# Optimization experiments

Hardware: AMD Instinct MI355X
Metric: run time of the kernel (lower is better)

## Reference

```python
import jax, jax.numpy as jnp
import numpy as np

B, S, E = 2, 2048, 1024
H, BLK = 16, 32
HD = E // H


def setup_inputs() -> dict:
    key = jax.random.key(0)
    ks = jax.random.split(key, 9)
    s = 1.0 / np.sqrt(E)
    return {
        "x": jax.random.normal(ks[0], (B, S, E), dtype=jnp.float32),
        "Wq": jax.random.normal(ks[1], (E, E), dtype=jnp.float32) * s,
        "bq": jnp.zeros((E,), dtype=jnp.float32),
        "Wk": jax.random.normal(ks[2], (E, E), dtype=jnp.float32) * s,
        "bk": jnp.zeros((E,), dtype=jnp.float32),
        "Wv": jax.random.normal(ks[3], (E, E), dtype=jnp.float32) * s,
        "bv": jnp.zeros((E,), dtype=jnp.float32),
        "Wo": jax.random.normal(ks[4], (E, E), dtype=jnp.float32) * s,
        "bo": jnp.zeros((E,), dtype=jnp.float32),
    }


def reference(x, Wq, bq, Wk, bk, Wv, bv, Wo, bo):
    b, s, e = x.shape
    # projections (torch Linear: x @ W.T + b), split heads -> [b, h, s, hd]
    def proj(W, bias):
        return (x @ W.T + bias).reshape(b, s, H, HD).transpose(0, 2, 1, 3)

    q = proj(Wq, bq)
    k = proj(Wk, bk)
    v = proj(Wv, bv)

    scale = 1.0 / np.sqrt(HD)
    scores = jnp.einsum("bhqd,bhkd->bhqk", q, k) * scale  # [b,h,s,s]

    # block-causal mask: query block i attends to all key blocks j <= i
    idx = jnp.arange(s)
    allowed = (idx[None, :] // BLK) <= (idx[:, None] // BLK)  # [s, s]
    scores = jnp.where(allowed[None, None], scores, jnp.float32(-1e9))

    probs = jax.nn.softmax(scores, axis=-1)
    attn = jnp.einsum("bhqk,bhkd->bhqd", probs, v)  # [b,h,s,hd]
    out = attn.transpose(0, 2, 1, 3).reshape(b, s, e)
    return out @ Wo.T + bo
```

## Files before the change

### kernel.cpp

```cpp
#include <hip/hip_runtime.h>
#include <hip/hip_bf16.h>
#include <stdint.h>

#define BATCH 2
#define S_LEN 2048
#define EMB   1024
#define NHEAD 16
#define HDIM  64

typedef __attribute__((ext_vector_type(8)))  __bf16 bf16x8;
typedef __attribute__((ext_vector_type(4)))  __bf16 bf16x4;
typedef __attribute__((ext_vector_type(4)))  float  f32x4;
typedef __attribute__((ext_vector_type(16))) float  f32x16;

#define ZERO16 ((f32x16){0.f,0.f,0.f,0.f,0.f,0.f,0.f,0.f,0.f,0.f,0.f,0.f,0.f,0.f,0.f,0.f})
#define SM_SCALE_LOG2 0.18033688011112042f

static __device__ __forceinline__ void gload_lds16(const void* g, void* l) {
    __builtin_amdgcn_global_load_lds(
        (__attribute__((address_space(1))) void*)g,
        (__attribute__((address_space(3))) void*)l,
        16, 0, 0);
}

__global__ void f2b_all(const float* __restrict__ x,
                        const float* __restrict__ Wq, const float* __restrict__ Wk,
                        const float* __restrict__ Wv, const float* __restrict__ Wo,
                        __bf16* __restrict__ xb,
                        __bf16* __restrict__ wqb, __bf16* __restrict__ wkb,
                        __bf16* __restrict__ wvb, __bf16* __restrict__ wob) {
    int i = blockIdx.x * blockDim.x + threadIdx.x;
    const float* s;
    __bf16* d;
    int off;
    if (i < (1 << 20)) {
        s = x; d = xb; off = i;
    } else {
        int r   = i - (1 << 20);
        int seg = r >> 18;
        off = r & ((1 << 18) - 1);
        s = seg == 0 ? Wq : seg == 1 ? Wk : seg == 2 ? Wv : Wo;
        d = seg == 0 ? wqb : seg == 1 ? wkb : seg == 2 ? wvb : wob;
    }
    float4 v = reinterpret_cast<const float4*>(s)[off];
    bf16x4 o = { (__bf16)v.x, (__bf16)v.y, (__bf16)v.z, (__bf16)v.w };
    reinterpret_cast<bf16x4*>(d)[off] = o;
}

__global__ __launch_bounds__(256)
void gemm_o64(const __bf16* __restrict__ A, const __bf16* __restrict__ W,
              const float* __restrict__ bias, float* __restrict__ out,
              int M, int N, int K) {
    __shared__ __align__(16) __bf16 As[2][128 * 32];
    __shared__ __align__(16) __bf16 Bs[2][64 * 32];

    const int t    = threadIdx.x;
    const int w    = t >> 6;
    const int lane = t & 63;
    const int m0   = blockIdx.y * 128;
    const int n0   = blockIdx.x * 64;
    const int wr   = w * 32;
    const int fr   = lane & 15;
    const int kg   = (lane >> 4) * 8;

    f32x4 acc[2][4];
#pragma unroll
    for (int i = 0; i < 2; ++i)
#pragma unroll
        for (int n = 0; n < 4; ++n) acc[i][n] = (f32x4){0.f, 0.f, 0.f, 0.f};

    auto stage = [&](int kt, int buf) {
#pragma unroll
        for (int i = 0; i < 2; ++i) {
            int chunk = i * 256 + t;
            int row   = chunk >> 2;
            int col   = (chunk & 3) * 8;
            gload_lds16(A + (size_t)(m0 + row) * K + kt + col,
                        (char*)&As[buf][0] + i * 4096 + w * 1024);
        }
        {
            int row = t >> 2;
            int col = (t & 3) * 8;
            gload_lds16(W + (size_t)(n0 + row) * K + kt + col,
                        (char*)&Bs[buf][0] + w * 1024);
        }
    };

    stage(0, 0);
    __syncthreads();

    const int NK = K / 32;
    for (int k6 = 0; k6 < NK; ++k6) {
        const int cur = k6 & 1;
        if (k6 + 1 < NK) stage((k6 + 1) * 32, cur ^ 1);

        bf16x8 af[2], bfv[4];
#pragma unroll
        for (int m = 0; m < 2; ++m)
            af[m] = *(const bf16x8*)&As[cur][(wr + m * 16 + fr) * 32 + kg];
#pragma unroll
        for (int n = 0; n < 4; ++n)
            bfv[n] = *(const bf16x8*)&Bs[cur][(n * 16 + fr) * 32 + kg];
#pragma unroll
        for (int m = 0; m < 2; ++m)
#pragma unroll
            for (int n = 0; n < 4; ++n)
                acc[m][n] = __builtin_amdgcn_mfma_f32_16x16x32_bf16(
                    af[m], bfv[n], acc[m][n], 0, 0, 0);
        __syncthreads();
    }

    const int rbase = (lane >> 4) * 4;
#pragma unroll
    for (int m = 0; m < 2; ++m) {
#pragma unroll
        for (int n = 0; n < 4; ++n) {
            int col  = n0 + n * 16 + fr;
            float bv = bias[col];
#pragma unroll
            for (int jj = 0; jj < 4; ++jj) {
                int row = m0 + wr + m * 16 + rbase + jj;
                out[(size_t)row * N + col] = acc[m][n][jj] + bv;
            }
        }
    }
}

__global__ __launch_bounds__(256)
void gemm_qkv(const __bf16* __restrict__ xb,
              const __bf16* __restrict__ Wqb, const __bf16* __restrict__ Wkb,
              const __bf16* __restrict__ Wvb,
              const float* __restrict__ bqp, const float* __restrict__ bkp,
              const float* __restrict__ bvp,
              __bf16* __restrict__ Qo, __bf16* __restrict__ Ko,
              __bf16* __restrict__ VTo, int K) {
    __shared__ __align__(16) __bf16 As[2][128 * 32];
    __shared__ __align__(16) __bf16 Bs[2][128 * 32];

    const int which = blockIdx.x >> 3;
    const int xx    = blockIdx.x & 7;

    const __bf16* Ap;
    const __bf16* Wp;
    int m0, n0;
    if (which == 2) {
        Ap = Wvb; Wp = xb;
        m0 = xx * 128;
        n0 = blockIdx.y * 128;
    } else {
        Ap = xb; Wp = (which == 0) ? Wqb : Wkb;
        m0 = blockIdx.y * 128;
        n0 = xx * 128;
    }
    const float* bias = which == 0 ? bqp : which == 1 ? bkp : bvp;

    const int t    = threadIdx.x;
    const int w    = t >> 6;
    const int lane = t & 63;
    const int wr   = (w >> 1) * 64;
    const int wc   = (w & 1) * 64;
    const int fr   = lane & 15;
    const int kg   = (lane >> 4) * 8;

    f32x4 acc[4][4];
#pragma unroll
    for (int i = 0; i < 4; ++i)
#pragma unroll
        for (int j = 0; j < 4; ++j) acc[i][j] = (f32x4){0.f, 0.f, 0.f, 0.f};

    auto stage = [&](int kt, int buf) {
#pragma unroll
        for (int i = 0; i < 2; ++i) {
            int chunk = i * 256 + t;
            int row   = chunk >> 2;
            int col   = (chunk & 3) * 8;
            gload_lds16(Ap + (size_t)(m0 + row) * K + kt + col,
                        (char*)&As[buf][0] + i * 4096 + w * 1024);
            gload_lds16(Wp + (size_t)(n0 + row) * K + kt + col,
                        (char*)&Bs[buf][0] + i * 4096 + w * 1024);
        }
    };

    stage(0, 0);
    __syncthreads();

    const int NK = K / 32;
    for (int k6 = 0; k6 < NK; ++k6) {
        const int cur = k6 & 1;
        if (k6 + 1 < NK) stage((k6 + 1) * 32, cur ^ 1);

        bf16x8 af[4], bfv[4];
#pragma unroll
        for (int m = 0; m < 4; ++m)
            af[m] = *(const bf16x8*)&As[cur][(wr + m * 16 + fr) * 32 + kg];
#pragma unroll
        for (int n = 0; n < 4; ++n)
            bfv[n] = *(const bf16x8*)&Bs[cur][(wc + n * 16 + fr) * 32 + kg];
#pragma unroll
        for (int m = 0; m < 4; ++m)
#pragma unroll
            for (int n = 0; n < 4; ++n)
                acc[m][n] = __builtin_amdgcn_mfma_f32_16x16x32_bf16(
                    af[m], bfv[n], acc[m][n], 0, 0, 0);
        __syncthreads();
    }

    const int rbase = (lane >> 4) * 4;
    if (which == 2) {
#pragma unroll
        for (int m = 0; m < 4; ++m) {
#pragma unroll
            for (int n = 0; n < 4; ++n) {
                int col = n0 + wc + n * 16 + fr;
                int b   = col >> 11, s = col & (S_LEN - 1);
#pragma unroll
                for (int jj = 0; jj < 4; ++jj) {
                    int row = m0 + wr + m * 16 + rbase + jj;
                    int hh  = row >> 6, d = row & (HDIM - 1);
                    float v = acc[m][n][jj] + bias[row];
                    VTo[(((size_t)(b * NHEAD + hh)) * HDIM + d) * S_LEN + s] = (__bf16)v;
                }
            }
        }
    } else {
        __bf16* outp = (which == 0) ? Qo : Ko;
#pragma unroll
        for (int m = 0; m < 4; ++m) {
#pragma unroll
            for (int n = 0; n < 4; ++n) {
                int col  = n0 + wc + n * 16 + fr;
                float bv = bias[col];
#pragma unroll
                for (int jj = 0; jj < 4; ++jj) {
                    int row = m0 + wr + m * 16 + rbase + jj;
                    float v = acc[m][n][jj] + bv;
                    int b = row >> 11, s = row & (S_LEN - 1);
                    int hh = col >> 6, d = col & (HDIM - 1);
                    outp[(((size_t)(b * NHEAD + hh)) * S_LEN + s) * HDIM + d] = (__bf16)v;
                }
            }
        }
    }
}

__global__ __launch_bounds__(512, 4)
void attn10_kernel(const __bf16* __restrict__ Q, const __bf16* __restrict__ Kv,
                   const __bf16* __restrict__ VT, __bf16* __restrict__ out) {
    __shared__ __align__(16) char smem[51200];
    __bf16* Kt0 = (__bf16*)smem;
    __bf16* Vt  = (__bf16*)(smem + 32768);
    float*  bc  = (float*)(smem + 49152);

    const int t    = threadIdx.x;
    const int w8   = t >> 6;
    const int lane = t & 63;
    const int h    = lane >> 5;
    const int q32  = lane & 31;
    const int j    = w8 & 3;
    const int h2   = w8 >> 2;
    const int bh   = blockIdx.x;
    const int yy   = blockIdx.y;
    const int qt   = (yy < 8) ? (15 - yy) : (yy - 8);
    const int qb   = 4 * qt + j;
    const int C    = qt + 1;

    const __bf16* Qp  = Q  + (size_t)bh * S_LEN * HDIM;
    const __bf16* Kp  = Kv + (size_t)bh * S_LEN * HDIM;
    const __bf16* VTp = VT + (size_t)bh * HDIM * S_LEN;

    const int qrow = qb * 32 + q32;

    bf16x8 qreg[4];
#pragma unroll
    for (int ks = 0; ks < 4; ++ks)
        qreg[ks] = *(const bf16x8*)&Qp[(size_t)qrow * HDIM + 16 * ks + 8 * h];

    f32x16 oacc0 = ZERO16, oacc1 = ZERO16;
    float mrun = -1e30f, lrun = 0.f;

    {
#pragma unroll
        for (int i = 0; i < 2; ++i) {
            int c16 = i * 512 + t;
            int key = c16 >> 3;
            int d0  = ((c16 & 7) ^ (key & 7)) * 8;
            gload_lds16(Kp + (size_t)key * HDIM + d0, (char*)Kt0 + c16 * 16);
        }
        __syncthreads();
    }

    for (int c = 0; c < C; ++c) {
        const int cur = c & 1;
        {
            const int kb = c * 128;
#pragma unroll
            for (int i = 0; i < 2; ++i) {
                int c16 = i * 512 + t;
                int d   = c16 >> 4;
                int o   = c16 & 15;
                gload_lds16(VTp + (size_t)d * S_LEN + kb + ((o ^ (d & 7)) * 8),
                            (char*)Vt + c16 * 16);
            }
        }
        if (c + 1 < C) {
            const int kb = (c + 1) * 128;
#pragma unroll
            for (int i = 0; i < 2; ++i) {
                int c16 = i * 512 + t;
                int key = c16 >> 3;
                int d0  = ((c16 & 7) ^ (key & 7)) * 8;
                gload_lds16(Kp + (size_t)(kb + key) * HDIM + d0,
                            (char*)Kt0 + (cur ^ 1) * 16384 + c16 * 16);
            }
        }

        const int  g0 = 4 * c + 2 * h2;
        const bool w0 = (g0 <= qb);
        const bool w1 = (g0 + 1 <= qb);
        const int  kl0 = 64 * h2;
        const __bf16* Ktc = Kt0 + cur * 8192;

        unsigned L[4], H[4];
        if (w0) {
            f32x16 sac = ZERO16;
            __builtin_amdgcn_s_setprio(1);
#pragma unroll
            for (int ks = 0; ks < 4; ++ks) {
                bf16x8 kf = *(const bf16x8*)&Ktc[(kl0 + q32) * 64 +
                                ((16 * ks + 8 * h) ^ ((q32 & 7) << 3))];
                sac = __builtin_amdgcn_mfma_f32_32x32x16_bf16(kf, qreg[ks], sac, 0, 0, 0);
            }
            __builtin_amdgcn_s_setprio(0);

            float rmax = sac[0];
#pragma unroll
            for (int r = 1; r < 16; ++r) rmax = fmaxf(rmax, sac[r]);
            float pmax = rmax * SM_SCALE_LOG2;
            pmax = fmaxf(pmax, __shfl_xor(pmax, 32));

            if (__any(pmax > mrun + 8.f)) {
                float mnew = fmaxf(mrun, pmax);
                float fac  = exp2f(mrun - mnew);
                mrun = mnew;
                lrun *= fac;
                bc[w8 * 32 + q32] = fac;
                asm volatile("s_waitcnt lgkmcnt(0)" ::: "memory");
                __builtin_amdgcn_sched_barrier(0);
#pragma unroll
                for (int q2 = 0; q2 < 4; ++q2) {
                    f32x4 fv = *(const f32x4*)&bc[w8 * 32 + 8 * q2 + 4 * h];
#pragma unroll
                    for (int jj = 0; jj < 4; ++jj) {
                        oacc0[4 * q2 + jj] *= fv[jj];
                        oacc1[4 * q2 + jj] *= fv[jj];
                    }
                }
            }

            float ps = 0.f;
#pragma unroll
            for (int r = 0; r < 16; ++r) {
                float pv = exp2f(__builtin_fmaf(sac[r], SM_SCALE_LOG2, -mrun));
                ps += pv;
                sac[r] = pv;
            }
            ps += __shfl_xor(ps, 32);
            lrun += ps;

#pragma unroll
            for (int g = 0; g < 4; ++g) {
                asm("v_cvt_pk_bf16_f32 %0, %1, %2"
                    : "=v"(L[g]) : "v"(sac[4 * g]), "v"(sac[4 * g + 1]));
                asm("v_cvt_pk_bf16_f32 %0, %1, %2"
                    : "=v"(H[g]) : "v"(sac[4 * g + 2]), "v"(sac[4 * g + 3]));
            }
        }

        __syncthreads();

        if (w0) {
            __builtin_amdgcn_s_setprio(1);
#pragma unroll
            for (int s2 = 0; s2 < 2; ++s2) {
                unsigned a0 = L[2 * s2], b0 = L[2 * s2 + 1];
                unsigned a1 = H[2 * s2], b1 = H[2 * s2 + 1];
                asm("v_permlane32_swap_b32 %0, %1" : "+v"(a0), "+v"(b0));
                asm("v_permlane32_swap_b32 %0, %1" : "+v"(a1), "+v"(b1));
                unsigned wvw[4] = { a0, a1, b0, b1 };
                bf16x8 pa = *(bf16x8*)wvw;

                const int klb = kl0 + 16 * s2 + 8 * h;
#pragma unroll
                for (int n = 0; n < 2; ++n) {
                    int d = 32 * n + q32;
                    bf16x8 vf = *(const bf16x8*)&Vt[d * 128 +
                                    (klb ^ ((d & 7) << 3))];
                    if (n == 0)
                        oacc0 = __builtin_amdgcn_mfma_f32_32x32x16_bf16(pa, vf, oacc0, 0, 0, 0);
                    else
                        oacc1 = __builtin_amdgcn_mfma_f32_32x32x16_bf16(pa, vf, oacc1, 0, 0, 0);
                }
            }
            __builtin_amdgcn_s_setprio(0);
        }

        if (w1) {
            const int kl1 = kl0 + 32;
            f32x16 sac = ZERO16;
            __builtin_amdgcn_s_setprio(1);
#pragma unroll
            for (int ks = 0; ks < 4; ++ks) {
                bf16x8 kf = *(const bf16x8*)&Ktc[(kl1 + q32) * 64 +
                                ((16 * ks + 8 * h) ^ ((q32 & 7) << 3))];
                sac = __builtin_amdgcn_mfma_f32_32x32x16_bf16(kf, qreg[ks], sac, 0, 0, 0);
            }
            __builtin_amdgcn_s_setprio(0);

            float rmax = sac[0];
#pragma unroll
            for (int r = 1; r < 16; ++r) rmax = fmaxf(rmax, sac[r]);
            float pmax = rmax * SM_SCALE_LOG2;
            pmax = fmaxf(pmax, __shfl_xor(pmax, 32));

            if (__any(pmax > mrun + 8.f)) {
                float mnew = fmaxf(mrun, pmax);
                float fac  = exp2f(mrun - mnew);
                mrun = mnew;
                lrun *= fac;
                bc[w8 * 32 + q32] = fac;
                asm volatile("s_waitcnt lgkmcnt(0)" ::: "memory");
                __builtin_amdgcn_sched_barrier(0);
#pragma unroll
                for (int q2 = 0; q2 < 4; ++q2) {
                    f32x4 fv = *(const f32x4*)&bc[w8 * 32 + 8 * q2 + 4 * h];
#pragma unroll
                    for (int jj = 0; jj < 4; ++jj) {
                        oacc0[4 * q2 + jj] *= fv[jj];
                        oacc1[4 * q2 + jj] *= fv[jj];
                    }
                }
            }

            float ps = 0.f;
#pragma unroll
            for (int r = 0; r < 16; ++r) {
                float pv = exp2f(__builtin_fmaf(sac[r], SM_SCALE_LOG2, -mrun));
                ps += pv;
                sac[r] = pv;
            }
            ps += __shfl_xor(ps, 32);
            lrun += ps;

            unsigned L1[4], H1[4];
#pragma unroll
            for (int g = 0; g < 4; ++g) {
                asm("v_cvt_pk_bf16_f32 %0, %1, %2"
                    : "=v"(L1[g]) : "v"(sac[4 * g]), "v"(sac[4 * g + 1]));
                asm("v_cvt_pk_bf16_f32 %0, %1, %2"
                    : "=v"(H1[g]) : "v"(sac[4 * g + 2]), "v"(sac[4 * g + 3]));
            }

            __builtin_amdgcn_s_setprio(1);
#pragma unroll
            for (int s2 = 0; s2 < 2; ++s2) {
                unsigned a0 = L1[2 * s2], b0 = L1[2 * s2 + 1];
                unsigned a1 = H1[2 * s2], b1 = H1[2 * s2 + 1];
                asm("v_permlane32_swap_b32 %0, %1" : "+v"(a0), "+v"(b0));
                asm("v_permlane32_swap_b32 %0, %1" : "+v"(a1), "+v"(b1));
                unsigned wvw[4] = { a0, a1, b0, b1 };
                bf16x8 pa = *(bf16x8*)wvw;

                const int klb = kl1 + 16 * s2 + 8 * h;
#pragma unroll
                for (int n = 0; n < 2; ++n) {
                    int d = 32 * n + q32;
                    bf16x8 vf = *(const bf16x8*)&Vt[d * 128 +
                                    (klb ^ ((d & 7) << 3))];
                    if (n == 0)
                        oacc0 = __builtin_amdgcn_mfma_f32_32x32x16_bf16(pa, vf, oacc0, 0, 0, 0);
                    else
                        oacc1 = __builtin_amdgcn_mfma_f32_32x32x16_bf16(pa, vf, oacc1, 0, 0, 0);
                }
            }
            __builtin_amdgcn_s_setprio(0);
        }

        __syncthreads();
    }

    float* Oex = (float*)smem;
    float* MLm = (float*)(smem + 49152);
    float* MLl = (float*)(smem + 50176);

    if (h == 0) { MLm[w8 * 32 + q32] = mrun; MLl[w8 * 32 + q32] = lrun; }
    if (h2 == 1) {
        float* ob = Oex + j * 2048;
#pragma unroll
        for (int q2 = 0; q2 < 4; ++q2)
#pragma unroll
            for (int jj = 0; jj < 4; ++jj) {
                int r  = 4 * q2 + jj;
                int rl = 8 * q2 + 4 * h + jj;
                ob[rl * 64 + q32]      = oacc0[r];
                ob[rl * 64 + 32 + q32] = oacc1[r];
            }
    }
    __syncthreads();

    if (h2 == 0) {
        const int b = bh >> 4, hh = bh & (NHEAD - 1);
        __bf16* op = out + (size_t)b * S_LEN * EMB + hh * HDIM;
        const float* ob = Oex + j * 2048;
#pragma unroll
        for (int q2 = 0; q2 < 4; ++q2) {
            f32x4 ma4 = *(const f32x4*)&MLm[j * 32 + 8 * q2 + 4 * h];
            f32x4 mb4 = *(const f32x4*)&MLm[(j + 4) * 32 + 8 * q2 + 4 * h];
            f32x4 la4 = *(const f32x4*)&MLl[j * 32 + 8 * q2 + 4 * h];
            f32x4 lb4 = *(const f32x4*)&MLl[(j + 4) * 32 + 8 * q2 + 4 * h];
#pragma unroll
            for (int jj = 0; jj < 4; ++jj) {
                float ma = ma4[jj], mb = mb4[jj];
                float mst = fmaxf(ma, mb);
                float sa  = exp2f(ma - mst), sb = exp2f(mb - mst);
                float inv = 1.f / (la4[jj] * sa + lb4[jj] * sb);
                int r  = 4 * q2 + jj;
                int rl = 8 * q2 + 4 * h + jj;
                int row = qb * 32 + rl;
                float v0 = (oacc0[r] * sa + ob[rl * 64 + q32] * sb) * inv;
                float v1 = (oacc1[r] * sa + ob[rl * 64 + 32 + q32] * sb) * inv;
                op[(size_t)row * EMB + q32]      = (__bf16)v0;
                op[(size_t)row * EMB + 32 + q32] = (__bf16)v1;
            }
        }
    }
}

extern "C" void kernel_launch(void* const* d_in, const int* in_sizes, int n_in,
                              void* d_out, int out_size, void* d_ws, size_t ws_size,
                              hipStream_t stream) {
    const float* x  = (const float*)d_in[0];
    const float* Wq = (const float*)d_in[1];
    const float* bq = (const float*)d_in[2];
    const float* Wk = (const float*)d_in[3];
    const float* bk = (const float*)d_in[4];
    const float* Wv = (const float*)d_in[5];
    const float* bv = (const float*)d_in[6];
    const float* Wo = (const float*)d_in[7];
    const float* bo = (const float*)d_in[8];
    float* out = (float*)d_out;

    char* ws = (char*)d_ws;
    __bf16* xb  = (__bf16*)(ws + 0);
    __bf16* wqb = (__bf16*)(ws + 8388608);
    __bf16* wkb = (__bf16*)(ws + 10485760);
    __bf16* wvb = (__bf16*)(ws + 12582912);
    __bf16* wob = (__bf16*)(ws + 14680064);
    __bf16* Qb  = (__bf16*)(ws + 16777216);
    __bf16* Kb  = (__bf16*)(ws + 25165824);
    __bf16* VTb = (__bf16*)(ws + 33554432);
    __bf16* Ab  = (__bf16*)(ws + 41943040);

    const int M = BATCH * S_LEN;
    const int N = EMB;
    const int K = EMB;

    f2b_all<<<8192, 256, 0, stream>>>(x, Wq, Wk, Wv, Wo, xb, wqb, wkb, wvb, wob);

    gemm_qkv<<<dim3(24, 32), 256, 0, stream>>>(
        xb, wqb, wkb, wvb, bq, bk, bv, Qb, Kb, VTb, K);

    attn10_kernel<<<dim3(BATCH * NHEAD, 16), 512, 0, stream>>>(Qb, Kb, VTb, Ab);

    gemm_o64<<<dim3(16, M / 128), 256, 0, stream>>>(Ab, wob, bo, out, M, N, K);
}
```

Measured before the change: 120.0 us.

## Triple-buffer GEMM LDS staging with explicit vmcnt waits and XOR swizzle

Both projection GEMMs move from double to triple buffering. Loads are issued two k-tiles ahead, and each iteration waits on an explicit s_waitcnt vmcnt count followed by a single barrier, replacing the two __syncthreads per iteration. An XOR swizzle on the 16-byte column chunk, applied on the global-load side with a matching read offset, is meant to cut LDS bank conflicts on fragment reads. This uses more LDS per block, which can lower occupancy, and correctness depends on the hand-counted vmcnt values.

```diff
diff --git a/kernel.cpp b/kernel.cpp
--- a/kernel.cpp
+++ b/kernel.cpp
@@ -51,8 +51,8 @@
 void gemm_o64(const __bf16* __restrict__ A, const __bf16* __restrict__ W,
               const float* __restrict__ bias, float* __restrict__ out,
               int M, int N, int K) {
-    __shared__ __align__(16) __bf16 As[2][128 * 32];
-    __shared__ __align__(16) __bf16 Bs[2][64 * 32];
+    __shared__ __align__(16) __bf16 As[3][128 * 32];
+    __shared__ __align__(16) __bf16 Bs[3][64 * 32];
 
     const int t    = threadIdx.x;
     const int w    = t >> 6;
@@ -62,6 +62,7 @@
     const int wr   = w * 32;
     const int fr   = lane & 15;
     const int kg   = (lane >> 4) * 8;
+    const int swz  = kg ^ ((fr & 3) << 3);
 
     f32x4 acc[2][4];
 #pragma unroll
@@ -74,40 +75,49 @@
         for (int i = 0; i < 2; ++i) {
             int chunk = i * 256 + t;
             int row   = chunk >> 2;
-            int col   = (chunk & 3) * 8;
+            int col   = ((chunk & 3) ^ (row & 3)) * 8;
             gload_lds16(A + (size_t)(m0 + row) * K + kt + col,
                         (char*)&As[buf][0] + i * 4096 + w * 1024);
         }
         {
             int row = t >> 2;
-            int col = (t & 3) * 8;
+            int col = ((t & 3) ^ (row & 3)) * 8;
             gload_lds16(W + (size_t)(n0 + row) * K + kt + col,
                         (char*)&Bs[buf][0] + w * 1024);
         }
     };
 
     stage(0, 0);
-    __syncthreads();
+    stage(32, 1);
 
     const int NK = K / 32;
     for (int k6 = 0; k6 < NK; ++k6) {
-        const int cur = k6 & 1;
-        if (k6 + 1 < NK) stage((k6 + 1) * 32, cur ^ 1);
-
+        __builtin_amdgcn_s_barrier();
+        if (k6 + 2 < NK) {
+            stage((k6 + 2) * 32, (k6 + 2) % 3);
+            asm volatile("s_waitcnt vmcnt(6)" ::: "memory");
+        } else if (k6 + 1 < NK) {
+            asm volatile("s_waitcnt vmcnt(3)" ::: "memory");
+        } else {
+            asm volatile("s_waitcnt vmcnt(0)" ::: "memory");
+        }
+        __builtin_amdgcn_sched_barrier(0);
+
+        const __bf16* Acur = &As[k6 % 3][0];
+        const __bf16* Bcur = &Bs[k6 % 3][0];
         bf16x8 af[2], bfv[4];
 #pragma unroll
         for (int m = 0; m < 2; ++m)
-            af[m] = *(const bf16x8*)&As[cur][(wr + m * 16 + fr) * 32 + kg];
+            af[m] = *(const bf16x8*)&Acur[(wr + m * 16 + fr) * 32 + swz];
 #pragma unroll
         for (int n = 0; n < 4; ++n)
-            bfv[n] = *(const bf16x8*)&Bs[cur][(n * 16 + fr) * 32 + kg];
+            bfv[n] = *(const bf16x8*)&Bcur[(n * 16 + fr) * 32 + swz];
 #pragma unroll
         for (int m = 0; m < 2; ++m)
 #pragma unroll
             for (int n = 0; n < 4; ++n)
                 acc[m][n] = __builtin_amdgcn_mfma_f32_16x16x32_bf16(
                     af[m], bfv[n], acc[m][n], 0, 0, 0);
-        __syncthreads();
     }
 
     const int rbase = (lane >> 4) * 4;
@@ -134,8 +144,8 @@
               const float* __restrict__ bvp,
               __bf16* __restrict__ Qo, __bf16* __restrict__ Ko,
               __bf16* __restrict__ VTo, int K) {
-    __shared__ __align__(16) __bf16 As[2][128 * 32];
-    __shared__ __align__(16) __bf16 Bs[2][128 * 32];
+    __shared__ __align__(16) __bf16 As[3][128 * 32];
+    __shared__ __align__(16) __bf16 Bs[3][128 * 32];
 
     const int which = blockIdx.x >> 3;
     const int xx    = blockIdx.x & 7;
@@ -161,6 +171,7 @@
     const int wc   = (w & 1) * 64;
     const int fr   = lane & 15;
     const int kg   = (lane >> 4) * 8;
+    const int swz  = kg ^ ((fr & 3) << 3);
 
     f32x4 acc[4][4];
 #pragma unroll
@@ -173,7 +184,7 @@
         for (int i = 0; i < 2; ++i) {
             int chunk = i * 256 + t;
             int row   = chunk >> 2;
-            int col   = (chunk & 3) * 8;
+            int col   = ((chunk & 3) ^ (row & 3)) * 8;
             gload_lds16(Ap + (size_t)(m0 + row) * K + kt + col,
                         (char*)&As[buf][0] + i * 4096 + w * 1024);
             gload_lds16(Wp + (size_t)(n0 + row) * K + kt + col,
@@ -182,27 +193,36 @@
     };
 
     stage(0, 0);
-    __syncthreads();
+    stage(32, 1);
 
     const int NK = K / 32;
     for (int k6 = 0; k6 < NK; ++k6) {
-        const int cur = k6 & 1;
-        if (k6 + 1 < NK) stage((k6 + 1) * 32, cur ^ 1);
-
+        __builtin_amdgcn_s_barrier();
+        if (k6 + 2 < NK) {
+            stage((k6 + 2) * 32, (k6 + 2) % 3);
+            asm volatile("s_waitcnt vmcnt(8)" ::: "memory");
+        } else if (k6 + 1 < NK) {
+            asm volatile("s_waitcnt vmcnt(4)" ::: "memory");
+        } else {
+            asm volatile("s_waitcnt vmcnt(0)" ::: "memory");
+        }
+        __builtin_amdgcn_sched_barrier(0);
+
+        const __bf16* Acur = &As[k6 % 3][0];
+        const __bf16* Bcur = &Bs[k6 % 3][0];
         bf16x8 af[4], bfv[4];
 #pragma unroll
         for (int m = 0; m < 4; ++m)
-            af[m] = *(const bf16x8*)&As[cur][(wr + m * 16 + fr) * 32 + kg];
+            af[m] = *(const bf16x8*)&Acur[(wr + m * 16 + fr) * 32 + swz];
 #pragma unroll
         for (int n = 0; n < 4; ++n)
-            bfv[n] = *(const bf16x8*)&Bs[cur][(wc + n * 16 + fr) * 32 + kg];
+            bfv[n] = *(const bf16x8*)&Bcur[(wc + n * 16 + fr) * 32 + swz];
 #pragma unroll
         for (int m = 0; m < 4; ++m)
 #pragma unroll
             for (int n = 0; n < 4; ++n)
                 acc[m][n] = __builtin_amdgcn_mfma_f32_16x16x32_bf16(
                     af[m], bfv[n], acc[m][n], 0, 0, 0);
-        __syncthreads();
     }
 
     const int rbase = (lane >> 4) * 4;
```

New measurement: 122.0 us. No clear change (+1.6%).

## Fuse Q and K projections into one block sharing the x tile

Applied to the files above, without the earlier changes.

Q and K projection blocks now share a single staged x tile and compute two accumulator sets against Wq and Wk, so x is loaded from global memory once for both. V blocks stay separate, which makes the grid uneven: 8 fused Q/K blocks carry double the work of the 8 V blocks. This cuts x reloads and the block count from 768 to 512. In exchange, register use doubles for the accumulators and LDS grows, which can lower occupancy and leave load imbalance between fused and V blocks.

```diff
diff --git a/kernel.cpp b/kernel.cpp
--- a/kernel.cpp
+++ b/kernel.cpp
@@ -127,32 +127,33 @@
 }
 
 __global__ __launch_bounds__(256)
-void gemm_qkv(const __bf16* __restrict__ xb,
-              const __bf16* __restrict__ Wqb, const __bf16* __restrict__ Wkb,
-              const __bf16* __restrict__ Wvb,
-              const float* __restrict__ bqp, const float* __restrict__ bkp,
-              const float* __restrict__ bvp,
-              __bf16* __restrict__ Qo, __bf16* __restrict__ Ko,
-              __bf16* __restrict__ VTo, int K) {
+void gemm_qkv2(const __bf16* __restrict__ xb,
+               const __bf16* __restrict__ Wqb, const __bf16* __restrict__ Wkb,
+               const __bf16* __restrict__ Wvb,
+               const float* __restrict__ bqp, const float* __restrict__ bkp,
+               const float* __restrict__ bvp,
+               __bf16* __restrict__ Qo, __bf16* __restrict__ Ko,
+               __bf16* __restrict__ VTo, int K) {
     __shared__ __align__(16) __bf16 As[2][128 * 32];
-    __shared__ __align__(16) __bf16 Bs[2][128 * 32];
-
-    const int which = blockIdx.x >> 3;
-    const int xx    = blockIdx.x & 7;
+    __shared__ __align__(16) __bf16 B0s[2][128 * 32];
+    __shared__ __align__(16) __bf16 B1s[2][128 * 32];
+
+    const bool isV = (blockIdx.x >= 8);
+    const int  xx  = blockIdx.x & 7;
 
     const __bf16* Ap;
-    const __bf16* Wp;
+    const __bf16* W0;
+    const __bf16* W1 = Wkb;
     int m0, n0;
-    if (which == 2) {
-        Ap = Wvb; Wp = xb;
+    if (isV) {
+        Ap = Wvb; W0 = xb;
         m0 = xx * 128;
         n0 = blockIdx.y * 128;
     } else {
-        Ap = xb; Wp = (which == 0) ? Wqb : Wkb;
+        Ap = xb; W0 = Wqb;
         m0 = blockIdx.y * 128;
         n0 = xx * 128;
     }
-    const float* bias = which == 0 ? bqp : which == 1 ? bkp : bvp;
 
     const int t    = threadIdx.x;
     const int w    = t >> 6;
@@ -162,11 +163,14 @@
     const int fr   = lane & 15;
     const int kg   = (lane >> 4) * 8;
 
-    f32x4 acc[4][4];
+    f32x4 accq[4][4], acck[4][4];
 #pragma unroll
     for (int i = 0; i < 4; ++i)
 #pragma unroll
-        for (int j = 0; j < 4; ++j) acc[i][j] = (f32x4){0.f, 0.f, 0.f, 0.f};
+        for (int j = 0; j < 4; ++j) {
+            accq[i][j] = (f32x4){0.f, 0.f, 0.f, 0.f};
+            acck[i][j] = (f32x4){0.f, 0.f, 0.f, 0.f};
+        }
 
     auto stage = [&](int kt, int buf) {
 #pragma unroll
@@ -176,8 +180,11 @@
             int col   = (chunk & 3) * 8;
             gload_lds16(Ap + (size_t)(m0 + row) * K + kt + col,
                         (char*)&As[buf][0] + i * 4096 + w * 1024);
-            gload_lds16(Wp + (size_t)(n0 + row) * K + kt + col,
-                        (char*)&Bs[buf][0] + i * 4096 + w * 1024);
+            gload_lds16(W0 + (size_t)(n0 + row) * K + kt + col,
+                        (char*)&B0s[buf][0] + i * 4096 + w * 1024);
+            if (!isV)
+                gload_lds16(W1 + (size_t)(n0 + row) * K + kt + col,
+                            (char*)&B1s[buf][0] + i * 4096 + w * 1024);
         }
     };
 
@@ -189,24 +196,36 @@
         const int cur = k6 & 1;
         if (k6 + 1 < NK) stage((k6 + 1) * 32, cur ^ 1);
 
-        bf16x8 af[4], bfv[4];
+        bf16x8 af[4], b0v[4];
 #pragma unroll
         for (int m = 0; m < 4; ++m)
             af[m] = *(const bf16x8*)&As[cur][(wr + m * 16 + fr) * 32 + kg];
 #pragma unroll
         for (int n = 0; n < 4; ++n)
-            bfv[n] = *(const bf16x8*)&Bs[cur][(wc + n * 16 + fr) * 32 + kg];
+            b0v[n] = *(const bf16x8*)&B0s[cur][(wc + n * 16 + fr) * 32 + kg];
 #pragma unroll
         for (int m = 0; m < 4; ++m)
 #pragma unroll
             for (int n = 0; n < 4; ++n)
-                acc[m][n] = __builtin_amdgcn_mfma_f32_16x16x32_bf16(
-                    af[m], bfv[n], acc[m][n], 0, 0, 0);
+                accq[m][n] = __builtin_amdgcn_mfma_f32_16x16x32_bf16(
+                    af[m], b0v[n], accq[m][n], 0, 0, 0);
+        if (!isV) {
+            bf16x8 b1v[4];
+#pragma unroll
+            for (int n = 0; n < 4; ++n)
+                b1v[n] = *(const bf16x8*)&B1s[cur][(wc + n * 16 + fr) * 32 + kg];
+#pragma unroll
+            for (int m = 0; m < 4; ++m)
+#pragma unroll
+                for (int n = 0; n < 4; ++n)
+                    acck[m][n] = __builtin_amdgcn_mfma_f32_16x16x32_bf16(
+                        af[m], b1v[n], acck[m][n], 0, 0, 0);
+        }
         __syncthreads();
     }
 
     const int rbase = (lane >> 4) * 4;
-    if (which == 2) {
+    if (isV) {
 #pragma unroll
         for (int m = 0; m < 4; ++m) {
 #pragma unroll
@@ -217,26 +236,27 @@
                 for (int jj = 0; jj < 4; ++jj) {
                     int row = m0 + wr + m * 16 + rbase + jj;
                     int hh  = row >> 6, d = row & (HDIM - 1);
-                    float v = acc[m][n][jj] + bias[row];
+                    float v = accq[m][n][jj] + bvp[row];
                     VTo[(((size_t)(b * NHEAD + hh)) * HDIM + d) * S_LEN + s] = (__bf16)v;
                 }
             }
         }
     } else {
-        __bf16* outp = (which == 0) ? Qo : Ko;
 #pragma unroll
         for (int m = 0; m < 4; ++m) {
 #pragma unroll
             for (int n = 0; n < 4; ++n) {
                 int col  = n0 + wc + n * 16 + fr;
-                float bv = bias[col];
+                float bq = bqp[col];
+                float bk = bkp[col];
 #pragma unroll
                 for (int jj = 0; jj < 4; ++jj) {
                     int row = m0 + wr + m * 16 + rbase + jj;
-                    float v = acc[m][n][jj] + bv;
                     int b = row >> 11, s = row & (S_LEN - 1);
                     int hh = col >> 6, d = col & (HDIM - 1);
-                    outp[(((size_t)(b * NHEAD + hh)) * S_LEN + s) * HDIM + d] = (__bf16)v;
+                    size_t idx = (((size_t)(b * NHEAD + hh)) * S_LEN + s) * HDIM + d;
+                    Qo[idx] = (__bf16)(accq[m][n][jj] + bq);
+                    Ko[idx] = (__bf16)(acck[m][n][jj] + bk);
                 }
             }
         }
@@ -566,7 +586,7 @@
 
     f2b_all<<<8192, 256, 0, stream>>>(x, Wq, Wk, Wv, Wo, xb, wqb, wkb, wvb, wob);
 
-    gemm_qkv<<<dim3(24, 32), 256, 0, stream>>>(
+    gemm_qkv2<<<dim3(16, 32), 256, 0, stream>>>(
         xb, wqb, wkb, wvb, bq, bk, bv, Qb, Kb, VTb, K);
 
     attn10_kernel<<<dim3(BATCH * NHEAD, 16), 512, 0, stream>>>(Qb, Kb, VTb, Ab);
```

Result: slower. 153.7 us (+28.1%).
